# Kernel optimization log

Hardware: AMD Instinct MI355X
Metric: run time of the kernel (lower is better)

The kernel has to match this reference:

```python
import jax, jax.numpy as jnp
import numpy as np

N_NODES = 100000
N_EDGES = 1200000
F_IN, HID, LAT = 128, 64, 32
N_GRAPHS = 512
NEG_SLOPE = 0.2  # PyG GATConv default


def setup_inputs() -> dict:
    key = jax.random.key(0)
    ks = jax.random.split(key, 20)
    inp = {
        'x': jax.random.normal(ks[0], (N_NODES, F_IN), jnp.float32),
        'edge_index': jax.random.randint(ks[1], (2, N_EDGES), 0, N_NODES, jnp.int32),
        'batch': jnp.sort(jax.random.randint(ks[2], (N_NODES,), 0, N_GRAPHS, jnp.int32)),
    }
    # GAT layer params: W [in,out], a_src/a_dst [out], bias [out] (heads=1)
    dims = [(F_IN, HID), (HID, HID), (HID, HID)]
    for i, (din, dout) in enumerate(dims):
        s = 1.0 / np.sqrt(din)
        inp[f'W{i}'] = jax.random.uniform(ks[3 + 4 * i], (din, dout), jnp.float32, -s, s)
        inp[f'a_src{i}'] = jax.random.normal(ks[4 + 4 * i], (dout,), jnp.float32) * 0.1
        inp[f'a_dst{i}'] = jax.random.normal(ks[5 + 4 * i], (dout,), jnp.float32) * 0.1
        inp[f'b{i}'] = jnp.zeros((dout,), jnp.float32)
    s = 1.0 / np.sqrt(HID)
    inp['fc_W'] = jax.random.uniform(ks[15], (HID, LAT), jnp.float32, -s, s)
    inp['fc_b'] = jnp.zeros((LAT,), jnp.float32)
    return inp


def _gat_layer(x, src, dst, W, a_src, a_dst, b, n):
    h = x @ W                                   # [N, out]
    e = (h @ a_src)[src] + (h @ a_dst)[dst]     # [E+N] raw scores
    e = jnp.where(e > 0, e, NEG_SLOPE * e)      # LeakyReLU
    # segmented softmax over incoming edges of each dst (self-loops guarantee non-empty)
    m = jax.ops.segment_max(e, dst, num_segments=n)
    w = jnp.exp(e - m[dst])
    denom = jax.ops.segment_sum(w, dst, num_segments=n)
    alpha = w / denom[dst]
    out = jax.ops.segment_sum(h[src] * alpha[:, None], dst, num_segments=n)
    return out + b


def reference(x, edge_index, batch, W0, a_src0, a_dst0, b0, W1, a_src1, a_dst1, b1,
              W2, a_src2, a_dst2, b2, fc_W, fc_b):
    n = x.shape[0]
    loops = jnp.arange(n, dtype=edge_index.dtype)
    src = jnp.concatenate([edge_index[0], loops])  # add_self_loops=True
    dst = jnp.concatenate([edge_index[1], loops])
    for (W, a_s, a_d, b) in ((W0, a_src0, a_dst0, b0),
                             (W1, a_src1, a_dst1, b1),
                             (W2, a_src2, a_dst2, b2)):
        x = jax.nn.relu(_gat_layer(x, src, dst, W, a_s, a_d, b, n))
    # dropout is identity in eval mode
    sums = jax.ops.segment_sum(x, batch, num_segments=N_GRAPHS)
    cnt = jax.ops.segment_sum(jnp.ones((n,), x.dtype), batch, num_segments=N_GRAPHS)
    pooled = sums / jnp.maximum(cnt, 1.0)[:, None]  # global_mean_pool
    return pooled @ fc_W + fc_b
```

## Files before the change

### kernel.cpp

```cpp
#include <hip/hip_runtime.h>
#include <hip/hip_bf16.h>
#include <hip/hip_fp16.h>

#define NN 100000
#define NE 1200000
#define NG 512
#define NBK ((NN + 511) / 512)
#define CAP 8192
#define SBATCH 4096
#define EPB (SBATCH / 256)

__global__ void k_binitF(int* gcur) {
    int b = blockIdx.x * blockDim.x + threadIdx.x;
    if (b < NBK) gcur[b] = b * CAP;
}

__global__ __launch_bounds__(256) void k_sortA(
    const int* __restrict__ srcA, const int* __restrict__ dstA, int e,
    int* gcur, uint2* __restrict__ ebuf) {
    __shared__ int cnt[NBK];
    __shared__ int base[NBK];
    const int t = threadIdx.x;
    const int i0 = blockIdx.x * SBATCH;
    for (int b = t; b < NBK; b += 256) cnt[b] = 0;
    __syncthreads();
#pragma unroll
    for (int k = 0; k < EPB; ++k) {
        int i = i0 + k * 256 + t;
        if (i < e) atomicAdd(&cnt[dstA[i] >> 9], 1);
    }
    __syncthreads();
    for (int b = t; b < NBK; b += 256) {
        int c = cnt[b];
        base[b] = c ? atomicAdd(&gcur[b], c) : 0;
        cnt[b] = 0;
    }
    __syncthreads();
#pragma unroll
    for (int k = 0; k < EPB; ++k) {
        int i = i0 + k * 256 + t;
        if (i < e) {
            int d = dstA[i], s = srcA[i];
            int b = d >> 9;
            int off = atomicAdd(&cnt[b], 1);
            int slot = base[b] + off;
            if (slot < (b + 1) * CAP)
                ebuf[slot] = make_uint2((unsigned)s, (unsigned)d);
        }
    }
}

__global__ __launch_bounds__(256) void k_hist2(
    const uint2* __restrict__ ebuf, const int* __restrict__ gcur,
    int* __restrict__ cnt, int n) {
    __shared__ int c512[512];
    const int b = blockIdx.x;
    const int d0 = b << 9;
    const int hi = min(n - d0, 512);
    for (int j = threadIdx.x; j < 512; j += 256) c512[j] = 0;
    __syncthreads();
    const int beg = b * CAP, end = gcur[b];
    for (int i = beg + threadIdx.x; i < end; i += 256)
        atomicAdd(&c512[(int)ebuf[i].y - d0], 1);
    __syncthreads();
    for (int j = threadIdx.x; j < hi; j += 256) cnt[d0 + j] = c512[j] + 1;
}

__global__ void k_scan1(const int* __restrict__ cnt, int n, int* ex, int* blkSum) {
    __shared__ int s[1024];
    int i = blockIdx.x * 1024 + threadIdx.x;
    int v = (i < n) ? cnt[i] : 0;
    s[threadIdx.x] = v;
    __syncthreads();
    for (int off = 1; off < 1024; off <<= 1) {
        int t = (threadIdx.x >= off) ? s[threadIdx.x - off] : 0;
        __syncthreads();
        s[threadIdx.x] += t;
        __syncthreads();
    }
    if (i < n) ex[i] = s[threadIdx.x] - v;
    if (threadIdx.x == 1023) blkSum[blockIdx.x] = s[1023];
}

__global__ void k_scan2(const int* __restrict__ blkSum, int nb, int* blkOff, int* totalOut) {
    __shared__ int s[128];
    int t = threadIdx.x;
    int v = (t < nb) ? blkSum[t] : 0;
    s[t] = v;
    __syncthreads();
    for (int off = 1; off < 128; off <<= 1) {
        int x = (t >= off) ? s[t - off] : 0;
        __syncthreads();
        s[t] += x;
        __syncthreads();
    }
    if (t < nb) blkOff[t] = s[t] - v;
    if (t == 127) *totalOut = s[127];
}

__global__ void k_scan3(int* row_ptr, int* cursor, const int* __restrict__ blkOff, int n) {
    int i = blockIdx.x * blockDim.x + threadIdx.x;
    if (i < n) {
        int v = row_ptr[i] + blkOff[i >> 10];
        row_ptr[i] = v;
        cursor[i] = v;
    }
}

__global__ void k_sortB(const uint2* __restrict__ ebuf, const int* __restrict__ gcur,
                        int n, int* cursor, int* __restrict__ col) {
    int i = blockIdx.x * blockDim.x + threadIdx.x;
    const int total = NBK * CAP;
    if (i < total) {
        int b = i >> 13;
        if (i < gcur[b]) {
            uint2 r = ebuf[i];
            int pos = atomicAdd(&cursor[(int)r.y], 1);
            col[pos] = (int)r.x;
        }
    } else if (i < total + n) {
        int v = i - total;
        int pos = atomicAdd(&cursor[v], 1);
        col[pos] = v;
    }
}

template <int K, bool HIN>
__global__ __launch_bounds__(256) void k_gemm_att(
    const float* __restrict__ Xf, const __half* __restrict__ Xh,
    const float* __restrict__ W,
    const float* __restrict__ a_src, const float* __restrict__ a_dst,
    __half* __restrict__ H, float* __restrict__ ssrc, float* __restrict__ sdst, int n) {
    constexpr int KC = 64;
    constexpr int NC = K / KC;
    constexpr int XP = KC + 8;
    constexpr int WP = 68;
    __shared__ float Xs[64 * XP];
    __shared__ float Ws[KC * WP];
    const int tid = threadIdx.x;
    const int row0 = blockIdx.x * 64;
    const int tx = tid & 15, ty = tid >> 4;
    float acc[4][4] = {};

    for (int c = 0; c < NC; ++c) {
        if (c) __syncthreads();
        for (int i = tid; i < KC * 16; i += 256) {
            int k = i >> 4, c4 = i & 15;
            float4 v = reinterpret_cast<const float4*>(W + (size_t)(c * KC + k) * 64)[c4];
            *reinterpret_cast<float4*>(&Ws[k * WP + c4 * 4]) = v;
        }
        for (int i = tid; i < 64 * 16; i += 256) {
            int r = i >> 4, c4 = i & 15;
            int row = row0 + r;
            float4 v = make_float4(0.f, 0.f, 0.f, 0.f);
            if (row < n) {
                if constexpr (HIN) {
                    float2 raw = reinterpret_cast<const float2*>(Xh + (size_t)row * K + c * KC)[c4];
                    const __half2* ph = reinterpret_cast<const __half2*>(&raw);
                    float2 lo = __half22float2(ph[0]), hi = __half22float2(ph[1]);
                    v = make_float4(lo.x, lo.y, hi.x, hi.y);
                } else {
                    v = reinterpret_cast<const float4*>(Xf + (size_t)row * K + c * KC)[c4];
                }
            }
            *reinterpret_cast<float4*>(&Xs[r * XP + c4 * 4]) = v;
        }
        __syncthreads();

        for (int k = 0; k < KC; k += 4) {
            float4 xv[4], wv[4];
#pragma unroll
            for (int r = 0; r < 4; ++r)
                xv[r] = *reinterpret_cast<const float4*>(&Xs[(ty * 4 + r) * XP + k]);
#pragma unroll
            for (int j = 0; j < 4; ++j)
                wv[j] = *reinterpret_cast<const float4*>(&Ws[(k + j) * WP + tx * 4]);
#pragma unroll
            for (int r = 0; r < 4; ++r) {
                const float* xp = reinterpret_cast<const float*>(&xv[r]);
#pragma unroll
                for (int j = 0; j < 4; ++j) {
                    const float* wp = reinterpret_cast<const float*>(&wv[j]);
#pragma unroll
                    for (int cc = 0; cc < 4; ++cc) acc[r][cc] += xp[j] * wp[cc];
                }
            }
        }
    }

    float4 av = reinterpret_cast<const float4*>(a_src)[tx];
    float4 dv = reinterpret_cast<const float4*>(a_dst)[tx];
#pragma unroll
    for (int r = 0; r < 4; ++r) {
        int row = row0 + ty * 4 + r;
        if (row < n) {
            __half2 h01 = __floats2half2_rn(acc[r][0], acc[r][1]);
            __half2 h23 = __floats2half2_rn(acc[r][2], acc[r][3]);
            float2 packed;
            *reinterpret_cast<__half2*>(&packed.x) = h01;
            *reinterpret_cast<__half2*>(&packed.y) = h23;
            reinterpret_cast<float2*>(H + (size_t)row * 64)[tx] = packed;
            float ps = acc[r][0] * av.x + acc[r][1] * av.y + acc[r][2] * av.z + acc[r][3] * av.w;
            float pd = acc[r][0] * dv.x + acc[r][1] * dv.y + acc[r][2] * dv.z + acc[r][3] * dv.w;
#pragma unroll
            for (int off = 1; off < 16; off <<= 1) {
                ps += __shfl_xor(ps, off);
                pd += __shfl_xor(pd, off);
            }
            if (tx == 0) {
                ssrc[row] = ps;
                sdst[row] = pd;
            }
        }
    }
}

__global__ __launch_bounds__(256) void k_agg5(
    const float2* __restrict__ H2, const float* __restrict__ ssrc,
    const float* __restrict__ sdst, const int* __restrict__ row_ptr,
    const int* __restrict__ col, const float4* __restrict__ bias4,
    float2* __restrict__ Yh2, int n) {
    const int wave = threadIdx.x >> 6, lane = threadIdx.x & 63;
    const int hf = lane >> 5, hl = lane & 31;
    const int base = blockIdx.x * 8 + wave * 2;
    const int dst = base + hf;

    int beg = 0, end = 0;
    if (dst < n) { beg = row_ptr[dst]; end = row_ptr[dst + 1]; }
    int deg = end - beg;
    int dmax = max(deg, __shfl_xor(deg, 32));

    if (dmax <= 32) {
        float sd = (dst < n) ? sdst[dst] : 0.f;
        int s_l = 0;
        float e = -INFINITY;
        if (hl < deg) {
            s_l = col[beg + hl];
            e = ssrc[s_l] + sd;
            e = (e > 0.f) ? e : 0.2f * e;
        }
        float m = e;
#pragma unroll
        for (int off = 16; off; off >>= 1) m = fmaxf(m, __shfl_xor(m, off));
        float w_l = (hl < deg) ? __expf(e - m) : 0.f;
        float den = w_l;
#pragma unroll
        for (int off = 16; off; off >>= 1) den += __shfl_xor(den, off);

        const int grp = hl >> 4, fl = hl & 15;
        float4 acc = make_float4(0.f, 0.f, 0.f, 0.f);
        for (int jj = 0; jj < deg; jj += 4) {
            int j0 = jj + grp, j1 = jj + 2 + grp;
            int s0 = __shfl(s_l, hf * 32 + j0), s1 = __shfl(s_l, hf * 32 + j1);
            float w0 = __shfl(w_l, hf * 32 + j0), w1 = __shfl(w_l, hf * 32 + j1);
            if (j0 < deg) {
                float2 raw = H2[(size_t)s0 * 16 + fl];
                const __half2* ph = reinterpret_cast<const __half2*>(&raw);
                float2 lo = __half22float2(ph[0]), hi = __half22float2(ph[1]);
                acc.x += w0 * lo.x; acc.y += w0 * lo.y;
                acc.z += w0 * hi.x; acc.w += w0 * hi.y;
            }
            if (j1 < deg) {
                float2 raw = H2[(size_t)s1 * 16 + fl];
                const __half2* ph = reinterpret_cast<const __half2*>(&raw);
                float2 lo = __half22float2(ph[0]), hi = __half22float2(ph[1]);
                acc.x += w1 * lo.x; acc.y += w1 * lo.y;
                acc.z += w1 * hi.x; acc.w += w1 * hi.y;
            }
        }
        acc.x += __shfl_xor(acc.x, 16);
        acc.y += __shfl_xor(acc.y, 16);
        acc.z += __shfl_xor(acc.z, 16);
        acc.w += __shfl_xor(acc.w, 16);
        if (grp == 0 && dst < n) {
            float inv = 1.f / den;
            float4 b = bias4[fl];
            float ox = fmaxf(acc.x * inv + b.x, 0.f);
            float oy = fmaxf(acc.y * inv + b.y, 0.f);
            float oz = fmaxf(acc.z * inv + b.z, 0.f);
            float ow = fmaxf(acc.w * inv + b.w, 0.f);
            float2 packed;
            *reinterpret_cast<__half2*>(&packed.x) = __floats2half2_rn(ox, oy);
            *reinterpret_cast<__half2*>(&packed.y) = __floats2half2_rn(oz, ow);
            Yh2[(size_t)dst * 16 + fl] = packed;
        }
    } else {
        for (int h = 0; h < 2; ++h) {
            int d = base + h;
            if (d >= n) break;
            int bg = row_ptr[d], en = row_ptr[d + 1];
            float sdd = sdst[d];
            float m = -INFINITY, d2 = 0.f;
            for (int c = bg; c < en; c += 64) {
                int j = c + lane;
                float e = -INFINITY;
                if (j < en) {
                    e = ssrc[col[j]] + sdd;
                    e = (e > 0.f) ? e : 0.2f * e;
                }
                float cm = e;
#pragma unroll
                for (int off = 32; off; off >>= 1) cm = fmaxf(cm, __shfl_xor(cm, off));
                float nm = fmaxf(m, cm);
                float term = (j < en) ? __expf(e - nm) : 0.f;
#pragma unroll
                for (int off = 32; off; off >>= 1) term += __shfl_xor(term, off);
                d2 = d2 * __expf(m - nm) + term;
                m = nm;
            }
            const int g4 = lane >> 4, fl = lane & 15;
            float4 acc = make_float4(0.f, 0.f, 0.f, 0.f);
            for (int jj = 0; jj < en - bg; jj += 8) {
                int j0 = bg + jj + g4, j1 = bg + jj + 4 + g4;
                if (j0 < en) {
                    int s = col[j0];
                    float e = ssrc[s] + sdd;
                    e = (e > 0.f) ? e : 0.2f * e;
                    float w = __expf(e - m);
                    float2 raw = H2[(size_t)s * 16 + fl];
                    const __half2* ph = reinterpret_cast<const __half2*>(&raw);
                    float2 lo = __half22float2(ph[0]), hi = __half22float2(ph[1]);
                    acc.x += w * lo.x; acc.y += w * lo.y;
                    acc.z += w * hi.x; acc.w += w * hi.y;
                }
                if (j1 < en) {
                    int s = col[j1];
                    float e = ssrc[s] + sdd;
                    e = (e > 0.f) ? e : 0.2f * e;
                    float w = __expf(e - m);
                    float2 raw = H2[(size_t)s * 16 + fl];
                    const __half2* ph = reinterpret_cast<const __half2*>(&raw);
                    float2 lo = __half22float2(ph[0]), hi = __half22float2(ph[1]);
                    acc.x += w * lo.x; acc.y += w * lo.y;
                    acc.z += w * hi.x; acc.w += w * hi.y;
                }
            }
#pragma unroll
            for (int off = 16; off < 64; off <<= 1) {
                acc.x += __shfl_xor(acc.x, off);
                acc.y += __shfl_xor(acc.y, off);
                acc.z += __shfl_xor(acc.z, off);
                acc.w += __shfl_xor(acc.w, off);
            }
            if (g4 == 0) {
                float inv = 1.f / d2;
                float4 b = bias4[fl];
                float ox = fmaxf(acc.x * inv + b.x, 0.f);
                float oy = fmaxf(acc.y * inv + b.y, 0.f);
                float oz = fmaxf(acc.z * inv + b.z, 0.f);
                float ow = fmaxf(acc.w * inv + b.w, 0.f);
                float2 packed;
                *reinterpret_cast<__half2*>(&packed.x) = __floats2half2_rn(ox, oy);
                *reinterpret_cast<__half2*>(&packed.y) = __floats2half2_rn(oz, ow);
                Yh2[(size_t)d * 16 + fl] = packed;
            }
        }
    }
}

__global__ void k_gstart(const int* __restrict__ batch, int n, int* gs) {
    int g = blockIdx.x * blockDim.x + threadIdx.x;
    if (g > NG) return;
    int lo = 0, hi = n;
    while (lo < hi) {
        int mid = (lo + hi) >> 1;
        if (batch[mid] < g) lo = mid + 1; else hi = mid;
    }
    gs[g] = lo;
}

__global__ __launch_bounds__(256) void k_pool_fc(
    const float2* __restrict__ Yh2, const int* __restrict__ gs,
    const float* __restrict__ fcW, const float* __restrict__ fcb,
    float* __restrict__ out) {
    __shared__ float4 part[4][16];
    __shared__ float p[64];
    const int g = blockIdx.x, tid = threadIdx.x;
    const int wave = tid >> 6, lane = tid & 63;
    const int grp = lane >> 4, fl = lane & 15;
    const int b = gs[g], e = gs[g + 1];

    float4 acc = make_float4(0.f, 0.f, 0.f, 0.f);
    for (int r = b + wave * 4 + grp; r < e; r += 16) {
        float2 raw = Yh2[(size_t)r * 16 + fl];
        const __half2* ph = reinterpret_cast<const __half2*>(&raw);
        float2 lo = __half22float2(ph[0]), hi = __half22float2(ph[1]);
        acc.x += lo.x; acc.y += lo.y; acc.z += hi.x; acc.w += hi.y;
    }
#pragma unroll
    for (int off = 16; off < 64; off <<= 1) {
        acc.x += __shfl_xor(acc.x, off);
        acc.y += __shfl_xor(acc.y, off);
        acc.z += __shfl_xor(acc.z, off);
        acc.w += __shfl_xor(acc.w, off);
    }
    if (grp == 0) part[wave][fl] = acc;
    __syncthreads();
    if (tid < 16) {
        float4 s0 = part[0][tid], s1 = part[1][tid], s2 = part[2][tid], s3 = part[3][tid];
        float inv = 1.f / (float)((e - b) > 0 ? (e - b) : 1);
        p[tid * 4 + 0] = (s0.x + s1.x + s2.x + s3.x) * inv;
        p[tid * 4 + 1] = (s0.y + s1.y + s2.y + s3.y) * inv;
        p[tid * 4 + 2] = (s0.z + s1.z + s2.z + s3.z) * inv;
        p[tid * 4 + 3] = (s0.w + s1.w + s2.w + s3.w) * inv;
    }
    __syncthreads();
    if (tid < 32) {
        float accO = fcb[tid];
#pragma unroll
        for (int k = 0; k < 64; ++k) accO += p[k] * fcW[k * 32 + tid];
        out[g * 32 + tid] = accO;
    }
}

extern "C" void kernel_launch(void* const* d_in, const int* in_sizes, int n_in,
                              void* d_out, int out_size, void* d_ws, size_t ws_size,
                              hipStream_t stream) {
    const float* x = (const float*)d_in[0];
    const int* ei = (const int*)d_in[1];
    const int* batch = (const int*)d_in[2];
    const float* W0 = (const float*)d_in[3];
    const float* as0 = (const float*)d_in[4];
    const float* ad0 = (const float*)d_in[5];
    const float* b0 = (const float*)d_in[6];
    const float* W1 = (const float*)d_in[7];
    const float* as1 = (const float*)d_in[8];
    const float* ad1 = (const float*)d_in[9];
    const float* b1 = (const float*)d_in[10];
    const float* W2 = (const float*)d_in[11];
    const float* as2 = (const float*)d_in[12];
    const float* ad2 = (const float*)d_in[13];
    const float* b2 = (const float*)d_in[14];
    const float* fcW = (const float*)d_in[15];
    const float* fcb = (const float*)d_in[16];
    float* out = (float*)d_out;

    char* w = (char*)d_ws;
    auto alloc = [&](size_t bytes) {
        void* p = (void*)w;
        w += (bytes + 255) & ~(size_t)255;
        return p;
    };
    int* cnt_cursor = (int*)alloc((size_t)NN * 4);
    int* row_ptr = (int*)alloc((size_t)(NN + 1) * 4);
    int* blkSum = (int*)alloc(512);
    int* blkOff = (int*)alloc(512);
    int* gcur = (int*)alloc((size_t)NBK * 4);
    int* col = (int*)alloc((size_t)(NE + NN) * 4);
    int* gs = (int*)alloc((size_t)(NG + 1) * 4);
    uint2* ebuf = (uint2*)alloc((size_t)NBK * CAP * 8);
    __half* H = (__half*)alloc((size_t)NN * 64 * 2);
    __half* Y = (__half*)alloc((size_t)NN * 64 * 2);
    float* ssrc = (float*)alloc((size_t)NN * 4);
    float* sdst = (float*)alloc((size_t)NN * 4);

    const int* srcA = ei;
    const int* dstA = ei + NE;

    k_binitF<<<1, 256, 0, stream>>>(gcur);
    k_sortA<<<(NE + SBATCH - 1) / SBATCH, 256, 0, stream>>>(srcA, dstA, NE, gcur, ebuf);
    k_hist2<<<NBK, 256, 0, stream>>>(ebuf, gcur, cnt_cursor, NN);
    const int nb = (NN + 1023) / 1024;
    k_scan1<<<nb, 1024, 0, stream>>>(cnt_cursor, NN, row_ptr, blkSum);
    k_scan2<<<1, 128, 0, stream>>>(blkSum, nb, blkOff, row_ptr + NN);
    k_scan3<<<(NN + 255) / 256, 256, 0, stream>>>(row_ptr, cnt_cursor, blkOff, NN);
    k_sortB<<<(NBK * CAP + NN + 255) / 256, 256, 0, stream>>>(ebuf, gcur, NN, cnt_cursor, col);
    k_gstart<<<3, 256, 0, stream>>>(batch, NN, gs);

    const int gemm_grid = (NN + 63) / 64;
    const int agg_grid = (NN + 7) / 8;

    k_gemm_att<128, false><<<gemm_grid, 256, 0, stream>>>(x, nullptr, W0, as0, ad0,
                                                          H, ssrc, sdst, NN);
    k_agg5<<<agg_grid, 256, 0, stream>>>((const float2*)H, ssrc, sdst, row_ptr, col,
                                         (const float4*)b0, (float2*)Y, NN);
    k_gemm_att<64, true><<<gemm_grid, 256, 0, stream>>>(nullptr, Y, W1, as1, ad1,
                                                        H, ssrc, sdst, NN);
    k_agg5<<<agg_grid, 256, 0, stream>>>((const float2*)H, ssrc, sdst, row_ptr, col,
                                         (const float4*)b1, (float2*)Y, NN);
    k_gemm_att<64, true><<<gemm_grid, 256, 0, stream>>>(nullptr, Y, W2, as2, ad2,
                                                        H, ssrc, sdst, NN);
    k_agg5<<<agg_grid, 256, 0, stream>>>((const float2*)H, ssrc, sdst, row_ptr, col,
                                         (const float4*)b2, (float2*)Y, NN);

    k_pool_fc<<<NG, 256, 0, stream>>>((const float2*)Y, gs, fcW, fcb, out);
}
```

Baseline: 287.5 us.

## Fuse aggregation with next-layer GEMM and use shared-memory cursors in CSR fill

The layer-0/1 aggregation is now fused with the following layer's GEMM and attention-score projection. Each block aggregates 64 destination rows into shared memory and then multiplies them by the next W, which removes the Y round-trip through global memory and two kernel launches. H and the scores are double-buffered to avoid read/write races. The CSR fill now processes one bucket per block with per-row cursors in shared-memory atomics instead of global atomics, and places the self-loop first. The fused kernel uses fewer blocks (64 rows per block) and a serial 8-iteration aggregation loop per wave, which may reduce parallelism for latency hiding.

```diff
diff --git a/kernel.cpp b/kernel.cpp
--- a/kernel.cpp
+++ b/kernel.cpp
@@ -98,43 +98,37 @@
     if (t == 127) *totalOut = s[127];
 }
 
-__global__ void k_scan3(int* row_ptr, int* cursor, const int* __restrict__ blkOff, int n) {
+__global__ void k_scan3(int* row_ptr, const int* __restrict__ blkOff, int n) {
     int i = blockIdx.x * blockDim.x + threadIdx.x;
-    if (i < n) {
-        int v = row_ptr[i] + blkOff[i >> 10];
-        row_ptr[i] = v;
-        cursor[i] = v;
-    }
-}
-
-__global__ void k_sortB(const uint2* __restrict__ ebuf, const int* __restrict__ gcur,
-                        int n, int* cursor, int* __restrict__ col) {
-    int i = blockIdx.x * blockDim.x + threadIdx.x;
-    const int total = NBK * CAP;
-    if (i < total) {
-        int b = i >> 13;
-        if (i < gcur[b]) {
-            uint2 r = ebuf[i];
-            int pos = atomicAdd(&cursor[(int)r.y], 1);
-            col[pos] = (int)r.x;
-        }
-    } else if (i < total + n) {
-        int v = i - total;
-        int pos = atomicAdd(&cursor[v], 1);
-        col[pos] = v;
-    }
-}
-
-template <int K, bool HIN>
-__global__ __launch_bounds__(256) void k_gemm_att(
-    const float* __restrict__ Xf, const __half* __restrict__ Xh,
-    const float* __restrict__ W,
+    if (i < n) row_ptr[i] += blkOff[i >> 10];
+}
+
+__global__ __launch_bounds__(512) void k_sortB2(
+    const uint2* __restrict__ ebuf, const int* __restrict__ gcur,
+    const int* __restrict__ row_ptr, int n, int* __restrict__ col) {
+    __shared__ int cur[512];
+    const int b = blockIdx.x;
+    const int d0 = b << 9;
+    const int hi = min(n - d0, 512);
+    for (int j = threadIdx.x; j < hi; j += 512) {
+        int rp = row_ptr[d0 + j];
+        col[rp] = d0 + j;
+        cur[j] = rp + 1;
+    }
+    __syncthreads();
+    const int beg = b * CAP, end = gcur[b];
+    for (int i = beg + threadIdx.x; i < end; i += 512) {
+        uint2 r = ebuf[i];
+        int pos = atomicAdd(&cur[(int)r.y - d0], 1);
+        col[pos] = (int)r.x;
+    }
+}
+
+__global__ __launch_bounds__(256) void k_gemm0(
+    const float* __restrict__ Xf, const float* __restrict__ W,
     const float* __restrict__ a_src, const float* __restrict__ a_dst,
     __half* __restrict__ H, float* __restrict__ ssrc, float* __restrict__ sdst, int n) {
-    constexpr int KC = 64;
-    constexpr int NC = K / KC;
-    constexpr int XP = KC + 8;
-    constexpr int WP = 68;
+    constexpr int K = 128, KC = 64, NC = 2, XP = 72, WP = 68;
     __shared__ float Xs[64 * XP];
     __shared__ float Ws[KC * WP];
     const int tid = threadIdx.x;
@@ -153,16 +147,8 @@
             int r = i >> 4, c4 = i & 15;
             int row = row0 + r;
             float4 v = make_float4(0.f, 0.f, 0.f, 0.f);
-            if (row < n) {
-                if constexpr (HIN) {
-                    float2 raw = reinterpret_cast<const float2*>(Xh + (size_t)row * K + c * KC)[c4];
-                    const __half2* ph = reinterpret_cast<const __half2*>(&raw);
-                    float2 lo = __half22float2(ph[0]), hi = __half22float2(ph[1]);
-                    v = make_float4(lo.x, lo.y, hi.x, hi.y);
-                } else {
-                    v = reinterpret_cast<const float4*>(Xf + (size_t)row * K + c * KC)[c4];
-                }
-            }
+            if (row < n)
+                v = reinterpret_cast<const float4*>(Xf + (size_t)row * K + c * KC)[c4];
             *reinterpret_cast<float4*>(&Xs[r * XP + c4 * 4]) = v;
         }
         __syncthreads();
@@ -194,11 +180,9 @@
     for (int r = 0; r < 4; ++r) {
         int row = row0 + ty * 4 + r;
         if (row < n) {
-            __half2 h01 = __floats2half2_rn(acc[r][0], acc[r][1]);
-            __half2 h23 = __floats2half2_rn(acc[r][2], acc[r][3]);
             float2 packed;
-            *reinterpret_cast<__half2*>(&packed.x) = h01;
-            *reinterpret_cast<__half2*>(&packed.y) = h23;
+            *reinterpret_cast<__half2*>(&packed.x) = __floats2half2_rn(acc[r][0], acc[r][1]);
+            *reinterpret_cast<__half2*>(&packed.y) = __floats2half2_rn(acc[r][2], acc[r][3]);
             reinterpret_cast<float2*>(H + (size_t)row * 64)[tx] = packed;
             float ps = acc[r][0] * av.x + acc[r][1] * av.y + acc[r][2] * av.z + acc[r][3] * av.w;
             float pd = acc[r][0] * dv.x + acc[r][1] * dv.y + acc[r][2] * dv.z + acc[r][3] * dv.w;
@@ -210,6 +194,211 @@
             if (tx == 0) {
                 ssrc[row] = ps;
                 sdst[row] = pd;
+            }
+        }
+    }
+}
+
+__global__ __launch_bounds__(256) void k_fused(
+    const float2* __restrict__ H2, const float* __restrict__ ssrc_in,
+    const float* __restrict__ sdst_in, const int* __restrict__ row_ptr,
+    const int* __restrict__ col, const float4* __restrict__ bias4,
+    const float* __restrict__ W, const float* __restrict__ a_src,
+    const float* __restrict__ a_dst, __half* __restrict__ Hout,
+    float* __restrict__ ssrc_out, float* __restrict__ sdst_out, int n) {
+    constexpr int XP = 72, WP = 68;
+    __shared__ float Xs[64 * XP];
+    __shared__ float Ws[64 * WP];
+    const int tid = threadIdx.x;
+    const int row0 = blockIdx.x * 64;
+    const int wave = tid >> 6, lane = tid & 63;
+    const int hf = lane >> 5, hl = lane & 31;
+
+    for (int i = tid; i < 64 * 16; i += 256) {
+        int k = i >> 4, c4 = i & 15;
+        float4 v = reinterpret_cast<const float4*>(W)[i];
+        *reinterpret_cast<float4*>(&Ws[k * WP + c4 * 4]) = v;
+    }
+
+    for (int it = 0; it < 8; ++it) {
+        const int r2 = wave * 16 + it * 2;
+        const int dst = row0 + r2 + hf;
+        int beg = 0, end = 0;
+        if (dst < n) { beg = row_ptr[dst]; end = row_ptr[dst + 1]; }
+        int deg = end - beg;
+        int dmax = max(deg, __shfl_xor(deg, 32));
+
+        if (dmax <= 32) {
+            float sd = (dst < n) ? sdst_in[dst] : 0.f;
+            int s_l = 0;
+            float e = -INFINITY;
+            if (hl < deg) {
+                s_l = col[beg + hl];
+                e = ssrc_in[s_l] + sd;
+                e = (e > 0.f) ? e : 0.2f * e;
+            }
+            float m = e;
+#pragma unroll
+            for (int off = 16; off; off >>= 1) m = fmaxf(m, __shfl_xor(m, off));
+            float w_l = (hl < deg) ? __expf(e - m) : 0.f;
+            float den = w_l;
+#pragma unroll
+            for (int off = 16; off; off >>= 1) den += __shfl_xor(den, off);
+
+            const int grp = hl >> 4, fl = hl & 15;
+            float4 acc = make_float4(0.f, 0.f, 0.f, 0.f);
+            for (int jj = 0; jj < deg; jj += 4) {
+                int j0 = jj + grp, j1 = jj + 2 + grp;
+                int s0 = __shfl(s_l, hf * 32 + j0), s1 = __shfl(s_l, hf * 32 + j1);
+                float w0 = __shfl(w_l, hf * 32 + j0), w1 = __shfl(w_l, hf * 32 + j1);
+                if (j0 < deg) {
+                    float2 raw = H2[(size_t)s0 * 16 + fl];
+                    const __half2* ph = reinterpret_cast<const __half2*>(&raw);
+                    float2 lo = __half22float2(ph[0]), hi = __half22float2(ph[1]);
+                    acc.x += w0 * lo.x; acc.y += w0 * lo.y;
+                    acc.z += w0 * hi.x; acc.w += w0 * hi.y;
+                }
+                if (j1 < deg) {
+                    float2 raw = H2[(size_t)s1 * 16 + fl];
+                    const __half2* ph = reinterpret_cast<const __half2*>(&raw);
+                    float2 lo = __half22float2(ph[0]), hi = __half22float2(ph[1]);
+                    acc.x += w1 * lo.x; acc.y += w1 * lo.y;
+                    acc.z += w1 * hi.x; acc.w += w1 * hi.y;
+                }
+            }
+            acc.x += __shfl_xor(acc.x, 16);
+            acc.y += __shfl_xor(acc.y, 16);
+            acc.z += __shfl_xor(acc.z, 16);
+            acc.w += __shfl_xor(acc.w, 16);
+            if (grp == 0) {
+                float4 o = make_float4(0.f, 0.f, 0.f, 0.f);
+                if (dst < n) {
+                    float inv = 1.f / den;
+                    float4 b = bias4[fl];
+                    o.x = fmaxf(acc.x * inv + b.x, 0.f);
+                    o.y = fmaxf(acc.y * inv + b.y, 0.f);
+                    o.z = fmaxf(acc.z * inv + b.z, 0.f);
+                    o.w = fmaxf(acc.w * inv + b.w, 0.f);
+                }
+                *reinterpret_cast<float4*>(&Xs[(r2 + hf) * XP + fl * 4]) = o;
+            }
+        } else {
+            for (int h = 0; h < 2; ++h) {
+                int d = row0 + r2 + h;
+                int bg = 0, en = 0;
+                if (d < n) { bg = row_ptr[d]; en = row_ptr[d + 1]; }
+                float sdd = (d < n) ? sdst_in[d] : 0.f;
+                float m = -INFINITY, d2 = 0.f;
+                for (int c = bg; c < en; c += 64) {
+                    int j = c + lane;
+                    float e = -INFINITY;
+                    if (j < en) {
+                        e = ssrc_in[col[j]] + sdd;
+                        e = (e > 0.f) ? e : 0.2f * e;
+                    }
+                    float cm = e;
+#pragma unroll
+                    for (int off = 32; off; off >>= 1) cm = fmaxf(cm, __shfl_xor(cm, off));
+                    float nm = fmaxf(m, cm);
+                    float term = (j < en) ? __expf(e - nm) : 0.f;
+#pragma unroll
+                    for (int off = 32; off; off >>= 1) term += __shfl_xor(term, off);
+                    d2 = d2 * __expf(m - nm) + term;
+                    m = nm;
+                }
+                const int g4 = lane >> 4, fl = lane & 15;
+                float4 acc = make_float4(0.f, 0.f, 0.f, 0.f);
+                for (int jj = 0; jj < en - bg; jj += 8) {
+                    int j0 = bg + jj + g4, j1 = bg + jj + 4 + g4;
+                    if (j0 < en) {
+                        int s = col[j0];
+                        float e = ssrc_in[s] + sdd;
+                        e = (e > 0.f) ? e : 0.2f * e;
+                        float wgt = __expf(e - m);
+                        float2 raw = H2[(size_t)s * 16 + fl];
+                        const __half2* ph = reinterpret_cast<const __half2*>(&raw);
+                        float2 lo = __half22float2(ph[0]), hi = __half22float2(ph[1]);
+                        acc.x += wgt * lo.x; acc.y += wgt * lo.y;
+                        acc.z += wgt * hi.x; acc.w += wgt * hi.y;
+                    }
+                    if (j1 < en) {
+                        int s = col[j1];
+                        float e = ssrc_in[s] + sdd;
+                        e = (e > 0.f) ? e : 0.2f * e;
+                        float wgt = __expf(e - m);
+                        float2 raw = H2[(size_t)s * 16 + fl];
+                        const __half2* ph = reinterpret_cast<const __half2*>(&raw);
+                        float2 lo = __half22float2(ph[0]), hi = __half22float2(ph[1]);
+                        acc.x += wgt * lo.x; acc.y += wgt * lo.y;
+                        acc.z += wgt * hi.x; acc.w += wgt * hi.y;
+                    }
+                }
+#pragma unroll
+                for (int off = 16; off < 64; off <<= 1) {
+                    acc.x += __shfl_xor(acc.x, off);
+                    acc.y += __shfl_xor(acc.y, off);
+                    acc.z += __shfl_xor(acc.z, off);
+                    acc.w += __shfl_xor(acc.w, off);
+                }
+                if (g4 == 0) {
+                    float4 o = make_float4(0.f, 0.f, 0.f, 0.f);
+                    if (d < n) {
+                        float inv = 1.f / d2;
+                        float4 b = bias4[fl];
+                        o.x = fmaxf(acc.x * inv + b.x, 0.f);
+                        o.y = fmaxf(acc.y * inv + b.y, 0.f);
+                        o.z = fmaxf(acc.z * inv + b.z, 0.f);
+                        o.w = fmaxf(acc.w * inv + b.w, 0.f);
+                    }
+                    *reinterpret_cast<float4*>(&Xs[(r2 + h) * XP + fl * 4]) = o;
+                }
+            }
+        }
+    }
+    __syncthreads();
+
+    const int tx = tid & 15, ty = tid >> 4;
+    float acc[4][4] = {};
+    for (int k = 0; k < 64; k += 4) {
+        float4 xv[4], wv[4];
+#pragma unroll
+        for (int r = 0; r < 4; ++r)
+            xv[r] = *reinterpret_cast<const float4*>(&Xs[(ty * 4 + r) * XP + k]);
+#pragma unroll
+        for (int j = 0; j < 4; ++j)
+            wv[j] = *reinterpret_cast<const float4*>(&Ws[(k + j) * WP + tx * 4]);
+#pragma unroll
+        for (int r = 0; r < 4; ++r) {
+            const float* xp = reinterpret_cast<const float*>(&xv[r]);
+#pragma unroll
+            for (int j = 0; j < 4; ++j) {
+                const float* wp = reinterpret_cast<const float*>(&wv[j]);
+#pragma unroll
+                for (int cc = 0; cc < 4; ++cc) acc[r][cc] += xp[j] * wp[cc];
+            }
+        }
+    }
+
+    float4 av = reinterpret_cast<const float4*>(a_src)[tx];
+    float4 dv = reinterpret_cast<const float4*>(a_dst)[tx];
+#pragma unroll
+    for (int r = 0; r < 4; ++r) {
+        int row = row0 + ty * 4 + r;
+        if (row < n) {
+            float2 packed;
+            *reinterpret_cast<__half2*>(&packed.x) = __floats2half2_rn(acc[r][0], acc[r][1]);
+            *reinterpret_cast<__half2*>(&packed.y) = __floats2half2_rn(acc[r][2], acc[r][3]);
+            reinterpret_cast<float2*>(Hout + (size_t)row * 64)[tx] = packed;
+            float ps = acc[r][0] * av.x + acc[r][1] * av.y + acc[r][2] * av.z + acc[r][3] * av.w;
+            float pd = acc[r][0] * dv.x + acc[r][1] * dv.y + acc[r][2] * dv.z + acc[r][3] * dv.w;
+#pragma unroll
+            for (int off = 1; off < 16; off <<= 1) {
+                ps += __shfl_xor(ps, off);
+                pd += __shfl_xor(pd, off);
+            }
+            if (tx == 0) {
+                ssrc_out[row] = ps;
+                sdst_out[row] = pd;
             }
         }
     }
@@ -316,23 +505,23 @@
                     int s = col[j0];
                     float e = ssrc[s] + sdd;
                     e = (e > 0.f) ? e : 0.2f * e;
-                    float w = __expf(e - m);
+                    float wgt = __expf(e - m);
                     float2 raw = H2[(size_t)s * 16 + fl];
                     const __half2* ph = reinterpret_cast<const __half2*>(&raw);
                     float2 lo = __half22float2(ph[0]), hi = __half22float2(ph[1]);
-                    acc.x += w * lo.x; acc.y += w * lo.y;
-                    acc.z += w * hi.x; acc.w += w * hi.y;
+                    acc.x += wgt * lo.x; acc.y += wgt * lo.y;
+                    acc.z += wgt * hi.x; acc.w += wgt * hi.y;
                 }
                 if (j1 < en) {
                     int s = col[j1];
                     float e = ssrc[s] + sdd;
                     e = (e > 0.f) ? e : 0.2f * e;
-                    float w = __expf(e - m);
+                    float wgt = __expf(e - m);
                     float2 raw = H2[(size_t)s * 16 + fl];
                     const __half2* ph = reinterpret_cast<const __half2*>(&raw);
                     float2 lo = __half22float2(ph[0]), hi = __half22float2(ph[1]);
-                    acc.x += w * lo.x; acc.y += w * lo.y;
-                    acc.z += w * hi.x; acc.w += w * hi.y;
+                    acc.x += wgt * lo.x; acc.y += wgt * lo.y;
+                    acc.z += wgt * hi.x; acc.w += wgt * hi.y;
                 }
             }
 #pragma unroll
@@ -441,7 +630,7 @@
         w += (bytes + 255) & ~(size_t)255;
         return p;
     };
-    int* cnt_cursor = (int*)alloc((size_t)NN * 4);
+    int* cnt = (int*)alloc((size_t)NN * 4);
     int* row_ptr = (int*)alloc((size_t)(NN + 1) * 4);
     int* blkSum = (int*)alloc(512);
     int* blkOff = (int*)alloc(512);
@@ -449,38 +638,38 @@
     int* col = (int*)alloc((size_t)(NE + NN) * 4);
     int* gs = (int*)alloc((size_t)(NG + 1) * 4);
     uint2* ebuf = (uint2*)alloc((size_t)NBK * CAP * 8);
-    __half* H = (__half*)alloc((size_t)NN * 64 * 2);
+    __half* Ha = (__half*)alloc((size_t)NN * 64 * 2);
+    __half* Hb = (__half*)alloc((size_t)NN * 64 * 2);
     __half* Y = (__half*)alloc((size_t)NN * 64 * 2);
-    float* ssrc = (float*)alloc((size_t)NN * 4);
-    float* sdst = (float*)alloc((size_t)NN * 4);
+    float* ssA = (float*)alloc((size_t)NN * 4);
+    float* sdA = (float*)alloc((size_t)NN * 4);
+    float* ssB = (float*)alloc((size_t)NN * 4);
+    float* sdB = (float*)alloc((size_t)NN * 4);
 
     const int* srcA = ei;
     const int* dstA = ei + NE;
 
     k_binitF<<<1, 256, 0, stream>>>(gcur);
     k_sortA<<<(NE + SBATCH - 1) / SBATCH, 256, 0, stream>>>(srcA, dstA, NE, gcur, ebuf);
-    k_hist2<<<NBK, 256, 0, stream>>>(ebuf, gcur, cnt_cursor, NN);
+    k_hist2<<<NBK, 256, 0, stream>>>(ebuf, gcur, cnt, NN);
     const int nb = (NN + 1023) / 1024;
-    k_scan1<<<nb, 1024, 0, stream>>>(cnt_cursor, NN, row_ptr, blkSum);
+    k_scan1<<<nb, 1024, 0, stream>>>(cnt, NN, row_ptr, blkSum);
     k_scan2<<<1, 128, 0, stream>>>(blkSum, nb, blkOff, row_ptr + NN);
-    k_scan3<<<(NN + 255) / 256, 256, 0, stream>>>(row_ptr, cnt_cursor, blkOff, NN);
-    k_sortB<<<(NBK * CAP + NN + 255) / 256, 256, 0, stream>>>(ebuf, gcur, NN, cnt_cursor, col);
+    k_scan3<<<(NN + 255) / 256, 256, 0, stream>>>(row_ptr, blkOff, NN);
+    k_sortB2<<<NBK, 512, 0, stream>>>(ebuf, gcur, row_ptr, NN, col);
     k_gstart<<<3, 256, 0, stream>>>(batch, NN, gs);
 
-    const int gemm_grid = (NN + 63) / 64;
+    const int tile_grid = (NN + 63) / 64;
     const int agg_grid = (NN + 7) / 8;
 
-    k_gemm_att<128, false><<<gemm_grid, 256, 0, stream>>>(x, nullptr, W0, as0, ad0,
-                                                          H, ssrc, sdst, NN);
-    k_agg5<<<agg_grid, 256, 0, stream>>>((const float2*)H, ssrc, sdst, row_ptr, col,
-                                         (const float4*)b0, (float2*)Y, NN);
-    k_gemm_att<64, true><<<gemm_grid, 256, 0, stream>>>(nullptr, Y, W1, as1, ad1,
-                                                        H, ssrc, sdst, NN);
-    k_agg5<<<agg_grid, 256, 0, stream>>>((const float2*)H, ssrc, sdst, row_ptr, col,
-                                         (const float4*)b1, (float2*)Y, NN);
-    k_gemm_att<64, true><<<gemm_grid, 256, 0, stream>>>(nullptr, Y, W2, as2, ad2,
-                                                        H, ssrc, sdst, NN);
-    k_agg5<<<agg_grid, 256, 0, stream>>>((const float2*)H, ssrc, sdst, row_ptr, col,
+    k_gemm0<<<tile_grid, 256, 0, stream>>>(x, W0, as0, ad0, Ha, ssA, sdA, NN);
+    k_fused<<<tile_grid, 256, 0, stream>>>((const float2*)Ha, ssA, sdA, row_ptr, col,
+                                           (const float4*)b0, W1, as1, ad1,
+                                           Hb, ssB, sdB, NN);
+    k_fused<<<tile_grid, 256, 0, stream>>>((const float2*)Hb, ssB, sdB, row_ptr, col,
+                                           (const float4*)b1, W2, as2, ad2,
+                                           Ha, ssA, sdA, NN);
+    k_agg5<<<agg_grid, 256, 0, stream>>>((const float2*)Ha, ssA, sdA, row_ptr, col,
                                          (const float4*)b2, (float2*)Y, NN);
 
     k_pool_fc<<<NG, 256, 0, stream>>>((const float2*)Y, gs, fcW, fcb, out);
```

After: 319.5 us. 11.1% more time.

## Fuse edge bucketing with first GEMM and sort buckets with block-local shared cursors

Applied to the files above, without the earlier changes.

The first-layer GEMM is merged into the same launch as the edge-bucketing sort pass, with block ranges split by blockIdx, so the two independent stages overlap and one launch is saved. The GEMM K-chunk shrinks to 32 so both branches fit a shared-memory budget that allows more resident blocks. The CSR fill is rewritten to process one 512-node bucket per block using shared-memory cursors instead of global atomics, and the self-loop is written first. Separate H and score buffers are allocated, which costs extra workspace memory.

```diff
diff --git a/kernel.cpp b/kernel.cpp
--- a/kernel.cpp
+++ b/kernel.cpp
@@ -9,19 +9,21 @@
 #define CAP 8192
 #define SBATCH 4096
 #define EPB (SBATCH / 256)
+#define SA_BLOCKS ((NE + SBATCH - 1) / SBATCH)
+#define TILES ((NN + 63) / 64)
 
 __global__ void k_binitF(int* gcur) {
     int b = blockIdx.x * blockDim.x + threadIdx.x;
     if (b < NBK) gcur[b] = b * CAP;
 }
 
-__global__ __launch_bounds__(256) void k_sortA(
+__device__ __forceinline__ void sortA_body(
     const int* __restrict__ srcA, const int* __restrict__ dstA, int e,
-    int* gcur, uint2* __restrict__ ebuf) {
-    __shared__ int cnt[NBK];
-    __shared__ int base[NBK];
+    int* gcur, uint2* __restrict__ ebuf, int bid, int* smemInt) {
+    int* cnt = smemInt;
+    int* base = smemInt + NBK;
     const int t = threadIdx.x;
-    const int i0 = blockIdx.x * SBATCH;
+    const int i0 = bid * SBATCH;
     for (int b = t; b < NBK; b += 256) cnt[b] = 0;
     __syncthreads();
 #pragma unroll
@@ -98,47 +100,47 @@
     if (t == 127) *totalOut = s[127];
 }
 
-__global__ void k_scan3(int* row_ptr, int* cursor, const int* __restrict__ blkOff, int n) {
+__global__ void k_scan3(int* row_ptr, const int* __restrict__ blkOff, int n) {
     int i = blockIdx.x * blockDim.x + threadIdx.x;
-    if (i < n) {
-        int v = row_ptr[i] + blkOff[i >> 10];
-        row_ptr[i] = v;
-        cursor[i] = v;
-    }
-}
-
-__global__ void k_sortB(const uint2* __restrict__ ebuf, const int* __restrict__ gcur,
-                        int n, int* cursor, int* __restrict__ col) {
-    int i = blockIdx.x * blockDim.x + threadIdx.x;
-    const int total = NBK * CAP;
-    if (i < total) {
-        int b = i >> 13;
-        if (i < gcur[b]) {
-            uint2 r = ebuf[i];
-            int pos = atomicAdd(&cursor[(int)r.y], 1);
-            col[pos] = (int)r.x;
-        }
-    } else if (i < total + n) {
-        int v = i - total;
-        int pos = atomicAdd(&cursor[v], 1);
-        col[pos] = v;
-    }
-}
+    if (i < n) row_ptr[i] += blkOff[i >> 10];
+}
+
+__global__ __launch_bounds__(512) void k_sortB2(
+    const uint2* __restrict__ ebuf, const int* __restrict__ gcur,
+    const int* __restrict__ row_ptr, int n, int* __restrict__ col) {
+    __shared__ int cur[512];
+    const int b = blockIdx.x;
+    const int d0 = b << 9;
+    const int hi = min(n - d0, 512);
+    for (int j = threadIdx.x; j < hi; j += 512) {
+        int rp = row_ptr[d0 + j];
+        col[rp] = d0 + j;
+        cur[j] = rp + 1;
+    }
+    __syncthreads();
+    const int beg = b * CAP, end = gcur[b];
+    for (int i = beg + threadIdx.x; i < end; i += 512) {
+        uint2 r = ebuf[i];
+        int pos = atomicAdd(&cur[(int)r.y - d0], 1);
+        col[pos] = (int)r.x;
+    }
+}
+
+#define XP 36
+#define WP 68
+#define SMEM_FLOATS (64 * XP + 32 * WP)
 
 template <int K, bool HIN>
-__global__ __launch_bounds__(256) void k_gemm_att(
+__device__ __forceinline__ void gemm_body(
     const float* __restrict__ Xf, const __half* __restrict__ Xh,
     const float* __restrict__ W,
     const float* __restrict__ a_src, const float* __restrict__ a_dst,
-    __half* __restrict__ H, float* __restrict__ ssrc, float* __restrict__ sdst, int n) {
-    constexpr int KC = 64;
+    __half* __restrict__ H, float* __restrict__ ssrc, float* __restrict__ sdst,
+    int n, int tile, float* __restrict__ Xs, float* __restrict__ Ws) {
+    constexpr int KC = 32;
     constexpr int NC = K / KC;
-    constexpr int XP = KC + 8;
-    constexpr int WP = 68;
-    __shared__ float Xs[64 * XP];
-    __shared__ float Ws[KC * WP];
     const int tid = threadIdx.x;
-    const int row0 = blockIdx.x * 64;
+    const int row0 = tile * 64;
     const int tx = tid & 15, ty = tid >> 4;
     float acc[4][4] = {};
 
@@ -149,8 +151,8 @@
             float4 v = reinterpret_cast<const float4*>(W + (size_t)(c * KC + k) * 64)[c4];
             *reinterpret_cast<float4*>(&Ws[k * WP + c4 * 4]) = v;
         }
-        for (int i = tid; i < 64 * 16; i += 256) {
-            int r = i >> 4, c4 = i & 15;
+        for (int i = tid; i < 64 * 8; i += 256) {
+            int r = i >> 3, c4 = i & 7;
             int row = row0 + r;
             float4 v = make_float4(0.f, 0.f, 0.f, 0.f);
             if (row < n) {
@@ -194,11 +196,9 @@
     for (int r = 0; r < 4; ++r) {
         int row = row0 + ty * 4 + r;
         if (row < n) {
-            __half2 h01 = __floats2half2_rn(acc[r][0], acc[r][1]);
-            __half2 h23 = __floats2half2_rn(acc[r][2], acc[r][3]);
             float2 packed;
-            *reinterpret_cast<__half2*>(&packed.x) = h01;
-            *reinterpret_cast<__half2*>(&packed.y) = h23;
+            *reinterpret_cast<__half2*>(&packed.x) = __floats2half2_rn(acc[r][0], acc[r][1]);
+            *reinterpret_cast<__half2*>(&packed.y) = __floats2half2_rn(acc[r][2], acc[r][3]);
             reinterpret_cast<float2*>(H + (size_t)row * 64)[tx] = packed;
             float ps = acc[r][0] * av.x + acc[r][1] * av.y + acc[r][2] * av.z + acc[r][3] * av.w;
             float pd = acc[r][0] * dv.x + acc[r][1] * dv.y + acc[r][2] * dv.z + acc[r][3] * dv.w;
@@ -213,6 +213,32 @@
             }
         }
     }
+}
+
+__global__ __launch_bounds__(256) void k_g0sA(
+    const int* __restrict__ srcA, const int* __restrict__ dstA,
+    int* gcur, uint2* __restrict__ ebuf,
+    const float* __restrict__ Xf, const float* __restrict__ W,
+    const float* __restrict__ a_src, const float* __restrict__ a_dst,
+    __half* __restrict__ H, float* __restrict__ ssrc, float* __restrict__ sdst, int n) {
+    __shared__ float smem[SMEM_FLOATS];
+    if (blockIdx.x < SA_BLOCKS) {
+        sortA_body(srcA, dstA, NE, gcur, ebuf, blockIdx.x, reinterpret_cast<int*>(smem));
+    } else {
+        gemm_body<128, false>(Xf, nullptr, W, a_src, a_dst, H, ssrc, sdst, n,
+                              blockIdx.x - SA_BLOCKS, smem, smem + 64 * XP);
+    }
+}
+
+template <int K, bool HIN>
+__global__ __launch_bounds__(256) void k_gemm_att(
+    const float* __restrict__ Xf, const __half* __restrict__ Xh,
+    const float* __restrict__ W,
+    const float* __restrict__ a_src, const float* __restrict__ a_dst,
+    __half* __restrict__ H, float* __restrict__ ssrc, float* __restrict__ sdst, int n) {
+    __shared__ float smem[SMEM_FLOATS];
+    gemm_body<K, HIN>(Xf, Xh, W, a_src, a_dst, H, ssrc, sdst, n,
+                      blockIdx.x, smem, smem + 64 * XP);
 }
 
 __global__ __launch_bounds__(256) void k_agg5(
@@ -316,23 +342,23 @@
                     int s = col[j0];
                     float e = ssrc[s] + sdd;
                     e = (e > 0.f) ? e : 0.2f * e;
-                    float w = __expf(e - m);
+                    float wgt = __expf(e - m);
                     float2 raw = H2[(size_t)s * 16 + fl];
                     const __half2* ph = reinterpret_cast<const __half2*>(&raw);
                     float2 lo = __half22float2(ph[0]), hi = __half22float2(ph[1]);
-                    acc.x += w * lo.x; acc.y += w * lo.y;
-                    acc.z += w * hi.x; acc.w += w * hi.y;
+                    acc.x += wgt * lo.x; acc.y += wgt * lo.y;
+                    acc.z += wgt * hi.x; acc.w += wgt * hi.y;
                 }
                 if (j1 < en) {
                     int s = col[j1];
                     float e = ssrc[s] + sdd;
                     e = (e > 0.f) ? e : 0.2f * e;
-                    float w = __expf(e - m);
+                    float wgt = __expf(e - m);
                     float2 raw = H2[(size_t)s * 16 + fl];
                     const __half2* ph = reinterpret_cast<const __half2*>(&raw);
                     float2 lo = __half22float2(ph[0]), hi = __half22float2(ph[1]);
-                    acc.x += w * lo.x; acc.y += w * lo.y;
-                    acc.z += w * hi.x; acc.w += w * hi.y;
+                    acc.x += wgt * lo.x; acc.y += wgt * lo.y;
+                    acc.z += wgt * hi.x; acc.w += wgt * hi.y;
                 }
             }
 #pragma unroll
@@ -441,7 +467,7 @@
         w += (bytes + 255) & ~(size_t)255;
         return p;
     };
-    int* cnt_cursor = (int*)alloc((size_t)NN * 4);
+    int* cnt = (int*)alloc((size_t)NN * 4);
     int* row_ptr = (int*)alloc((size_t)(NN + 1) * 4);
     int* blkSum = (int*)alloc(512);
     int* blkOff = (int*)alloc(512);
@@ -449,38 +475,39 @@
     int* col = (int*)alloc((size_t)(NE + NN) * 4);
     int* gs = (int*)alloc((size_t)(NG + 1) * 4);
     uint2* ebuf = (uint2*)alloc((size_t)NBK * CAP * 8);
-    __half* H = (__half*)alloc((size_t)NN * 64 * 2);
+    __half* Ha = (__half*)alloc((size_t)NN * 64 * 2);
+    __half* Hb = (__half*)alloc((size_t)NN * 64 * 2);
     __half* Y = (__half*)alloc((size_t)NN * 64 * 2);
-    float* ssrc = (float*)alloc((size_t)NN * 4);
-    float* sdst = (float*)alloc((size_t)NN * 4);
+    float* ssA = (float*)alloc((size_t)NN * 4);
+    float* sdA = (float*)alloc((size_t)NN * 4);
+    float* ssB = (float*)alloc((size_t)NN * 4);
+    float* sdB = (float*)alloc((size_t)NN * 4);
 
     const int* srcA = ei;
     const int* dstA = ei + NE;
 
     k_binitF<<<1, 256, 0, stream>>>(gcur);
-    k_sortA<<<(NE + SBATCH - 1) / SBATCH, 256, 0, stream>>>(srcA, dstA, NE, gcur, ebuf);
-    k_hist2<<<NBK, 256, 0, stream>>>(ebuf, gcur, cnt_cursor, NN);
+    k_g0sA<<<SA_BLOCKS + TILES, 256, 0, stream>>>(srcA, dstA, gcur, ebuf,
+                                                  x, W0, as0, ad0, Ha, ssA, sdA, NN);
+    k_hist2<<<NBK, 256, 0, stream>>>(ebuf, gcur, cnt, NN);
     const int nb = (NN + 1023) / 1024;
-    k_scan1<<<nb, 1024, 0, stream>>>(cnt_cursor, NN, row_ptr, blkSum);
+    k_scan1<<<nb, 1024, 0, stream>>>(cnt, NN, row_ptr, blkSum);
     k_scan2<<<1, 128, 0, stream>>>(blkSum, nb, blkOff, row_ptr + NN);
-    k_scan3<<<(NN + 255) / 256, 256, 0, stream>>>(row_ptr, cnt_cursor, blkOff, NN);
-    k_sortB<<<(NBK * CAP + NN + 255) / 256, 256, 0, stream>>>(ebuf, gcur, NN, cnt_cursor, col);
+    k_scan3<<<(NN + 255) / 256, 256, 0, stream>>>(row_ptr, blkOff, NN);
+    k_sortB2<<<NBK, 512, 0, stream>>>(ebuf, gcur, row_ptr, NN, col);
     k_gstart<<<3, 256, 0, stream>>>(batch, NN, gs);
 
-    const int gemm_grid = (NN + 63) / 64;
     const int agg_grid = (NN + 7) / 8;
 
-    k_gemm_att<128, false><<<gemm_grid, 256, 0, stream>>>(x, nullptr, W0, as0, ad0,
-                                                          H, ssrc, sdst, NN);
-    k_agg5<<<agg_grid, 256, 0, stream>>>((const float2*)H, ssrc, sdst, row_ptr, col,
-                                         (const float4*)b0, (float2*)Y, NN);
-    k_gemm_att<64, true><<<gemm_grid, 256, 0, stream>>>(nullptr, Y, W1, as1, ad1,
-                                                        H, ssrc, sdst, NN);
-    k_agg5<<<agg_grid, 256, 0, stream>>>((const float2*)H, ssrc, sdst, row_ptr, col,
-                                         (const float4*)b1, (float2*)Y, NN);
-    k_gemm_att<64, true><<<gemm_grid, 256, 0, stream>>>(nullptr, Y, W2, as2, ad2,
-                                                        H, ssrc, sdst, NN);
-    k_agg5<<<agg_grid, 256, 0, stream>>>((const float2*)H, ssrc, sdst, row_ptr, col,
+    k_agg5<<<agg_grid, 256, 0, stream>>>((const float2*)Ha, ssA, sdA, row_ptr, col,
+                                         (const float4*)b0, (float2*)Hb, NN);
+    k_gemm_att<64, true><<<TILES, 256, 0, stream>>>(nullptr, Hb, W1, as1, ad1,
+                                                    Ha, ssB, sdB, NN);
+    k_agg5<<<agg_grid, 256, 0, stream>>>((const float2*)Ha, ssB, sdB, row_ptr, col,
+                                         (const float4*)b1, (float2*)Hb, NN);
+    k_gemm_att<64, true><<<TILES, 256, 0, stream>>>(nullptr, Hb, W2, as2, ad2,
+                                                    Ha, ssA, sdA, NN);
+    k_agg5<<<agg_grid, 256, 0, stream>>>((const float2*)Ha, ssA, sdA, row_ptr, col,
                                          (const float4*)b2, (float2*)Y, NN);
 
     k_pool_fc<<<NG, 256, 0, stream>>>((const float2*)Y, gs, fcW, fcb, out);
```

Measured after the change: 244.9 us. -14.8%, faster.
